# Optimization experiments

Hardware: AMD Instinct MI355X
Metric: run time of the kernel (lower is better)

The kernel has to match this reference:

```python
import jax, jax.numpy as jnp
import numpy as np
from jax import lax


def ternary_quant(w):
    # Layer-wise ternary quantization: alpha = mean(|w|), threshold = 0.001*alpha
    alpha = lax.stop_gradient(jnp.mean(jnp.abs(w)))
    thr = 0.001 * alpha
    q = jnp.where(w > thr, 1.0, jnp.where(w < -thr, -1.0, 0.0))
    return alpha * q


def setup_inputs() -> dict:
    key = jax.random.key(0)
    k1, k2, k3, k4, k5 = jax.random.split(key, 5)
    B, C, H, W = 32, 384, 64, 64
    fan_in = C * 3 * 3
    bound = 1.0 / np.sqrt(fan_in)  # torch Conv2d default init scale
    return {
        "x": jax.random.normal(k1, (B, C, H, W), dtype=jnp.float32),
        "weight": jax.random.uniform(k2, (C, C, 3, 3), dtype=jnp.float32, minval=-bound, maxval=bound),
        "bias": jax.random.uniform(k3, (C,), dtype=jnp.float32, minval=-bound, maxval=bound),
        "time_emb": jax.random.normal(k4, (B, 512), dtype=jnp.float32),
        "y": jax.random.randint(k5, (B,), 0, 1000, dtype=jnp.int64),
    }


def reference(x, weight, bias, time_emb, y):
    # time_emb and y are accepted but unused, matching Downsample.forward
    qw = ternary_quant(weight)
    out = lax.conv_general_dilated(
        x, qw,
        window_strides=(2, 2),
        padding=((1, 1), (1, 1)),
        dimension_numbers=("NCHW", "OIHW", "NCHW"),
    )
    return out + bias[None, :, None, None]
```

## Files before the change

### kernel.cpp

```cpp
#include <hip/hip_runtime.h>
#include <hip/hip_bf16.h>


#define CIN   384
#define HIN   64
#define WIN   64
#define OHW   32
#define KDIM  3456
#define NWELT 1327104
#define MDIM  32768

using bf16 = __hip_bfloat16;
typedef __attribute__((ext_vector_type(8))) short short8;
typedef __attribute__((ext_vector_type(4))) float floatx4;
typedef __attribute__((ext_vector_type(2))) unsigned short ushort2v;

#define AS1 __attribute__((address_space(1)))
#define AS3 __attribute__((address_space(3)))
#define DMA16(g, l) __builtin_amdgcn_global_load_lds((const AS1 void*)(g), (AS3 void*)(l), 16, 0, 0)

#define NPART  62
#define ZG_F   16
#define XN_OFF 256
#define WQ_OFF (256 + 100663296)

__global__ void absum_part(const float* __restrict__ w, float* __restrict__ ws) {
    const float4* w4 = (const float4*)w;
    float s = 0.f;
    for (int i = blockIdx.x * 256 + threadIdx.x; i < NWELT / 4; i += NPART * 256) {
        float4 v = w4[i];
        s += fabsf(v.x) + fabsf(v.y) + fabsf(v.z) + fabsf(v.w);
    }
    for (int off = 32; off; off >>= 1) s += __shfl_down(s, off, 64);
    __shared__ float red[4];
    if ((threadIdx.x & 63) == 0) red[threadIdx.x >> 6] = s;
    __syncthreads();
    if (threadIdx.x == 0) ws[2 + blockIdx.x] = red[0] + red[1] + red[2] + red[3];
}

__global__ void absum_final(float* __restrict__ ws) {
    if (threadIdx.x == 0) {
        float s = 0.f;
        for (int i = 0; i < NPART; ++i) s += ws[2 + i];
        float alpha = s * (1.0f / NWELT);
        ws[0] = alpha;
        ws[1] = 1e-3f * alpha;
        ws[ZG_F + 0] = 0.f; ws[ZG_F + 1] = 0.f;
        ws[ZG_F + 2] = 0.f; ws[ZG_F + 3] = 0.f;
    }
}

__global__ void quant_kernel(const float* __restrict__ w, const float* __restrict__ ws,
                             bf16* __restrict__ wq) {
    int j = blockIdx.x * 256 + threadIdx.x;
    if (j >= NWELT) return;
    float thr = ws[1];
    int o = j / KDIM;
    int rmd = j - o * KDIM;
    int khkw = rmd / 384;
    int c = rmd - khkw * 384;
    float v = w[((o * 384 + c) * 9) + khkw];
    float q = (v > thr) ? 1.f : ((v < -thr) ? -1.f : 0.f);
    wq[j] = __float2bfloat16(q);
}

__global__ void nhwc_kernel(const float* __restrict__ x, bf16* __restrict__ xn) {
    int nh = blockIdx.x;
    int n = nh >> 6, h = nh & 63;
    int c0 = blockIdx.y * 64;
    __shared__ bf16 tile[64][66];
    const float* src = x + ((n * CIN + c0) * HIN + h) * WIN;
    for (int i = 0; i < 4; ++i) {
        int s = threadIdx.x + i * 256;
        int cl = s >> 4, w4 = (s & 15) * 4;
        float4 v = *(const float4*)(src + cl * 4096 + w4);
        bf16 t0[2], t1[2];
        t0[0] = __float2bfloat16(v.x); t0[1] = __float2bfloat16(v.y);
        t1[0] = __float2bfloat16(v.z); t1[1] = __float2bfloat16(v.w);
        *(ushort2v*)&tile[cl][w4]     = *(ushort2v*)t0;
        *(ushort2v*)&tile[cl][w4 + 2] = *(ushort2v*)t1;
    }
    __syncthreads();
    bf16* dst = xn + ((size_t)(n * HIN + h) * WIN) * CIN + c0;
    for (int i = 0; i < 2; ++i) {
        int q = threadIdx.x + i * 256;
        int wc = q >> 3, c8 = (q & 7) * 8;
        bf16 tmp[8];
        #pragma unroll
        for (int j = 0; j < 8; ++j) tmp[j] = tile[c8 + j][wc];
        *(short8*)(dst + (size_t)wc * CIN + c8) = *(short8*)tmp;
    }
}

#define BM  128
#define BNO 128

__global__ __launch_bounds__(256) void conv_gemm(const bf16* __restrict__ xn,
                                                 const bf16* __restrict__ wq,
                                                 const float* __restrict__ ws,
                                                 const float* __restrict__ bias,
                                                 float* __restrict__ out,
                                                 const bf16* __restrict__ zg) {
    int m_base = blockIdx.x * BM;
    int o_base = blockIdx.y * BNO;
    __shared__ __align__(16) bf16 lW[BNO * 64];
    __shared__ __align__(16) bf16 lX[BM * 64];
    int tid = threadIdx.x;
    int lane = tid & 63;
    int wv = tid >> 6;
    int wo = (wv & 1) * 64;
    int wm = (wv >> 1) * 64;

    int g = (lane & 7) ^ (lane >> 3);
    const bf16* pw[4];
    const bf16* pxn[4];
    int oh2[4], ow2[4];
    bf16* ldsWb[4]; bf16* ldsXb[4];
    #pragma unroll
    for (int i = 0; i < 4; ++i) {
        int r = (wv * 4 + i) * 8 + (lane >> 3);
        ldsWb[i] = &lW[(wv * 4 + i) * 512];
        ldsXb[i] = &lX[(wv * 4 + i) * 512];
        pw[i] = wq + (size_t)(o_base + r) * KDIM + g * 8;
        int m = m_base + r;
        int n = m >> 10, oh = (m >> 5) & 31, ow = m & 31;
        pxn[i] = xn + (size_t)n * (HIN * WIN * CIN) + g * 8;
        oh2[i] = 2 * oh - 1;
        ow2[i] = 2 * ow - 1;
    }

    floatx4 acc[4][4];
    for (int i = 0; i < 4; ++i)
        for (int j = 0; j < 4; ++j)
            acc[i][j] = (floatx4){0.f, 0.f, 0.f, 0.f};

    for (int khkw = 0; khkw < 9; ++khkw) {
        int kh = khkw / 3, kw = khkw % 3;
        const bf16* pwk[4];
        const bf16* pxk[4];
        #pragma unroll
        for (int i = 0; i < 4; ++i) {
            pwk[i] = pw[i] + khkw * 384;
            int ih = oh2[i] + kh, iw = ow2[i] + kw;
            bool valid = (ih >= 0) & (iw >= 0);
            pxk[i] = valid ? pxn[i] + (ih * WIN + iw) * CIN : (const bf16*)0;
        }
        for (int cc = 0; cc < 6; ++cc) {
            int coff = cc * 64;
            #pragma unroll
            for (int i = 0; i < 4; ++i)
                DMA16(pwk[i] + coff, ldsWb[i]);
            #pragma unroll
            for (int i = 0; i < 4; ++i) {
                const bf16* p = pxk[i] ? pxk[i] + coff : zg;
                DMA16(p, ldsXb[i]);
            }
            __syncthreads();
            #pragma unroll
            for (int ks = 0; ks < 2; ++ks) {
                int oct = ((ks * 4 + (lane >> 4)) ^ (lane & 7)) * 8;
                short8 af[4], bfr[4];
                #pragma unroll
                for (int i = 0; i < 4; ++i)
                    af[i] = *(const short8*)(&lW[(wo + i * 16 + (lane & 15)) * 64 + oct]);
                #pragma unroll
                for (int j = 0; j < 4; ++j)
                    bfr[j] = *(const short8*)(&lX[(wm + j * 16 + (lane & 15)) * 64 + oct]);
                #pragma unroll
                for (int i = 0; i < 4; ++i)
                    #pragma unroll
                    for (int j = 0; j < 4; ++j)
                        acc[i][j] = __builtin_amdgcn_mfma_f32_16x16x32_bf16(af[i], bfr[j], acc[i][j], 0, 0, 0);
            }
            __syncthreads();
        }
    }

    float alpha = ws[0];
    int quad = lane >> 4, colm = lane & 15;
    for (int i = 0; i < 4; ++i) {
        for (int j = 0; j < 4; ++j) {
            int mm = m_base + wm + j * 16 + colm;
            int n = mm >> 10, oh = (mm >> 5) & 31, ow = mm & 31;
            for (int r = 0; r < 4; ++r) {
                int o = o_base + wo + i * 16 + quad * 4 + r;
                out[((n * 384 + o) * OHW + oh) * OHW + ow] = alpha * acc[i][j][r] + bias[o];
            }
        }
    }
}

extern "C" void kernel_launch(void* const* d_in, const int* in_sizes, int n_in,
                              void* d_out, int out_size, void* d_ws, size_t ws_size,
                              hipStream_t stream) {
    (void)in_sizes; (void)n_in; (void)out_size; (void)ws_size;
    const float* x    = (const float*)d_in[0];
    const float* w    = (const float*)d_in[1];
    const float* bias = (const float*)d_in[2];
    float* out = (float*)d_out;
    float* wsf = (float*)d_ws;
    bf16* xn = (bf16*)((char*)d_ws + XN_OFF);
    bf16* wq = (bf16*)((char*)d_ws + WQ_OFF);
    const bf16* zg = (const bf16*)(wsf + ZG_F);

    absum_part<<<NPART, 256, 0, stream>>>(w, wsf);
    absum_final<<<1, 64, 0, stream>>>(wsf);
    quant_kernel<<<(NWELT + 255) / 256, 256, 0, stream>>>(w, wsf, wq);
    nhwc_kernel<<<dim3(2048, 6), 256, 0, stream>>>(x, xn);
    conv_gemm<<<dim3(MDIM / BM, 384 / BNO), 256, 0, stream>>>(xn, wq, wsf, bias, out, zg);
}
```

Before: 427.7 us.

## Restructure conv GEMM into double-buffered 128x384 tile with interleaved DMA and MFMA

Each block of the implicit-GEMM conv kernel now covers all 384 output channels for 128 output pixels using 512 threads (8 waves), replacing the previous 128x128 tile grid. LDS is double-buffered, and global_load_lds prefetches of the next K-slice are interleaved with MFMA phases using explicit vmcnt waits, barriers and setprio. The aim is to reuse each input tile across all output channels, overlap memory traffic with compute, and reduce synchronisation stalls. In exchange it uses much more LDS per block and more accumulator registers, which can limit occupancy, and it depends on hand-tuned wait counts.

Result: no change. 426.3 us (-0.3%).

```diff
diff --git a/kernel.cpp b/kernel.cpp
--- a/kernel.cpp
+++ b/kernel.cpp
@@ -9,6 +9,7 @@
 #define KDIM  3456
 #define NWELT 1327104
 #define MDIM  32768
+#define NT    54
 
 using bf16 = __hip_bfloat16;
 typedef __attribute__((ext_vector_type(8))) short short8;
@@ -18,6 +19,12 @@
 #define AS1 __attribute__((address_space(1)))
 #define AS3 __attribute__((address_space(3)))
 #define DMA16(g, l) __builtin_amdgcn_global_load_lds((const AS1 void*)(g), (AS3 void*)(l), 16, 0, 0)
+
+#define EDGE(N) do { \
+    asm volatile("s_waitcnt vmcnt(" #N ")" ::: "memory"); \
+    __builtin_amdgcn_s_barrier(); \
+    __builtin_amdgcn_sched_barrier(0); \
+} while (0)
 
 #define NPART  62
 #define ZG_F   16
@@ -93,98 +100,257 @@
 }
 
 #define BM  128
-#define BNO 128
-
-__global__ __launch_bounds__(256) void conv_gemm(const bf16* __restrict__ xn,
-                                                 const bf16* __restrict__ wq,
-                                                 const float* __restrict__ ws,
-                                                 const float* __restrict__ bias,
-                                                 float* __restrict__ out,
-                                                 const bf16* __restrict__ zg) {
-    int m_base = blockIdx.x * BM;
-    int o_base = blockIdx.y * BNO;
-    __shared__ __align__(16) bf16 lW[BNO * 64];
-    __shared__ __align__(16) bf16 lX[BM * 64];
-    int tid = threadIdx.x;
-    int lane = tid & 63;
-    int wv = tid >> 6;
-    int wo = (wv & 1) * 64;
-    int wm = (wv >> 1) * 64;
-
-    int g = (lane & 7) ^ (lane >> 3);
-    const bf16* pw[4];
-    const bf16* pxn[4];
-    int oh2[4], ow2[4];
-    bf16* ldsWb[4]; bf16* ldsXb[4];
-    #pragma unroll
-    for (int i = 0; i < 4; ++i) {
-        int r = (wv * 4 + i) * 8 + (lane >> 3);
-        ldsWb[i] = &lW[(wv * 4 + i) * 512];
-        ldsXb[i] = &lX[(wv * 4 + i) * 512];
-        pw[i] = wq + (size_t)(o_base + r) * KDIM + g * 8;
-        int m = m_base + r;
+
+__global__ __launch_bounds__(512, 2) void conv_gemm(const bf16* __restrict__ xn,
+                                                    const bf16* __restrict__ wq,
+                                                    const float* __restrict__ ws,
+                                                    const float* __restrict__ bias,
+                                                    float* __restrict__ out,
+                                                    const bf16* __restrict__ zg) {
+    __shared__ __align__(16) bf16 lW[2][384 * 64];
+    __shared__ __align__(16) bf16 lX[2][128 * 64];
+    const int m_base = blockIdx.x * BM;
+    const int tid = threadIdx.x;
+    const int lane = tid & 63;
+    const int wv = tid >> 6;
+    const int io = wv & 3;
+    const int im = wv >> 2;
+    const int g = (lane & 7) ^ (lane >> 3);
+
+    const bf16* pw[2][3];
+    int wLoff[2][3];
+    #pragma unroll
+    for (int h = 0; h < 2; ++h)
+        #pragma unroll
+        for (int j = 0; j < 3; ++j) {
+            int rr = h * 192 + wv * 24 + j * 8;
+            pw[h][j] = wq + (size_t)(rr + (lane >> 3)) * KDIM + g * 8;
+            wLoff[h][j] = rr * 64;
+        }
+    const bf16* pxn[2];
+    int oh2[2], ow2[2], xLoff[2];
+    #pragma unroll
+    for (int h = 0; h < 2; ++h) {
+        int rr = h * 64 + wv * 8;
+        int m = m_base + rr + (lane >> 3);
         int n = m >> 10, oh = (m >> 5) & 31, ow = m & 31;
-        pxn[i] = xn + (size_t)n * (HIN * WIN * CIN) + g * 8;
-        oh2[i] = 2 * oh - 1;
-        ow2[i] = 2 * ow - 1;
-    }
-
-    floatx4 acc[4][4];
-    for (int i = 0; i < 4; ++i)
+        pxn[h] = xn + (size_t)n * (HIN * WIN * CIN) + g * 8;
+        oh2[h] = 2 * oh - 1;
+        ow2[h] = 2 * ow - 1;
+        xLoff[h] = rr * 64;
+    }
+
+    const int l15 = lane & 15, quad = lane >> 4, l7 = lane & 7;
+    const int octA = (quad ^ l7) * 8;
+    const int octB = ((4 + quad) ^ l7) * 8;
+    int aoff[2][3], boff[2][2];
+    #pragma unroll
+    for (int h = 0; h < 2; ++h)
+        #pragma unroll
+        for (int fo = 0; fo < 3; ++fo)
+            aoff[h][fo] = (h * 192 + io * 48 + fo * 16 + l15) * 64;
+    #pragma unroll
+    for (int h = 0; h < 2; ++h)
+        #pragma unroll
+        for (int fm = 0; fm < 2; ++fm)
+            boff[h][fm] = (h * 64 + im * 32 + fm * 16 + l15) * 64;
+
+    floatx4 acc[6][4];
+    #pragma unroll
+    for (int i = 0; i < 6; ++i)
+        #pragma unroll
         for (int j = 0; j < 4; ++j)
             acc[i][j] = (floatx4){0.f, 0.f, 0.f, 0.f};
 
-    for (int khkw = 0; khkw < 9; ++khkw) {
-        int kh = khkw / 3, kw = khkw % 3;
-        const bf16* pwk[4];
-        const bf16* pxk[4];
-        #pragma unroll
-        for (int i = 0; i < 4; ++i) {
-            pwk[i] = pw[i] + khkw * 384;
-            int ih = oh2[i] + kh, iw = ow2[i] + kw;
-            bool valid = (ih >= 0) & (iw >= 0);
-            pxk[i] = valid ? pxn[i] + (ih * WIN + iw) * CIN : (const bf16*)0;
-        }
-        for (int cc = 0; cc < 6; ++cc) {
-            int coff = cc * 64;
-            #pragma unroll
-            for (int i = 0; i < 4; ++i)
-                DMA16(pwk[i] + coff, ldsWb[i]);
-            #pragma unroll
-            for (int i = 0; i < 4; ++i) {
-                const bf16* p = pxk[i] ? pxk[i] + coff : zg;
-                DMA16(p, ldsXb[i]);
-            }
-            __syncthreads();
-            #pragma unroll
-            for (int ks = 0; ks < 2; ++ks) {
-                int oct = ((ks * 4 + (lane >> 4)) ^ (lane & 7)) * 8;
-                short8 af[4], bfr[4];
-                #pragma unroll
-                for (int i = 0; i < 4; ++i)
-                    af[i] = *(const short8*)(&lW[(wo + i * 16 + (lane & 15)) * 64 + oct]);
-                #pragma unroll
-                for (int j = 0; j < 4; ++j)
-                    bfr[j] = *(const short8*)(&lX[(wm + j * 16 + (lane & 15)) * 64 + oct]);
-                #pragma unroll
-                for (int i = 0; i < 4; ++i)
-                    #pragma unroll
-                    for (int j = 0; j < 4; ++j)
-                        acc[i][j] = __builtin_amdgcn_mfma_f32_16x16x32_bf16(af[i], bfr[j], acc[i][j], 0, 0, 0);
-            }
-            __syncthreads();
-        }
+    {
+        #pragma unroll
+        for (int j = 0; j < 3; ++j) DMA16(pw[0][j], &lW[0][wLoff[0][j]]);
+        {
+            int ih = oh2[0], iw = ow2[0];
+            const bf16* p = (ih >= 0 && iw >= 0) ? pxn[0] + (ih * WIN + iw) * CIN : zg;
+            DMA16(p, &lX[0][xLoff[0]]);
+        }
+        {
+            int ih = oh2[1], iw = ow2[1];
+            const bf16* p = (ih >= 0 && iw >= 0) ? pxn[1] + (ih * WIN + iw) * CIN : zg;
+            DMA16(p, &lX[0][xLoff[1]]);
+        }
+        #pragma unroll
+        for (int j = 0; j < 3; ++j) DMA16(pw[1][j], &lW[0][wLoff[1][j]]);
+        EDGE(4);
+    }
+
+    short8 af[2][3], bfl[2][2], bfh[2][2];
+
+    for (int t = 0; t < NT - 1; ++t) {
+        bf16* lWc = lW[t & 1];
+        bf16* lXc = lX[t & 1];
+        bf16* lWn = lW[(t & 1) ^ 1];
+        bf16* lXn = lX[(t & 1) ^ 1];
+        const int s = t + 1;
+        const int kk = s / 6, cs = s - kk * 6;
+        const int kh = kk / 3, kw = kk - kh * 3;
+        const int ws64 = s * 64;
+        const bf16* pxs[2];
+        #pragma unroll
+        for (int h = 0; h < 2; ++h) {
+            int ih = oh2[h] + kh, iw = ow2[h] + kw;
+            pxs[h] = (ih >= 0 && iw >= 0) ? pxn[h] + (ih * WIN + iw) * CIN + cs * 64 : zg;
+        }
+
+        #pragma unroll
+        for (int fo = 0; fo < 3; ++fo) {
+            af[0][fo] = *(const short8*)(lWc + aoff[0][fo] + octA);
+            af[1][fo] = *(const short8*)(lWc + aoff[0][fo] + octB);
+        }
+        #pragma unroll
+        for (int fm = 0; fm < 2; ++fm) {
+            bfl[0][fm] = *(const short8*)(lXc + boff[0][fm] + octA);
+            bfl[1][fm] = *(const short8*)(lXc + boff[0][fm] + octB);
+        }
+        #pragma unroll
+        for (int j = 0; j < 3; ++j) DMA16(pw[0][j] + ws64, lWn + wLoff[0][j]);
+        EDGE(6);
+        __builtin_amdgcn_s_setprio(1);
+        #pragma unroll
+        for (int ks = 0; ks < 2; ++ks)
+            #pragma unroll
+            for (int fo = 0; fo < 3; ++fo)
+                #pragma unroll
+                for (int fm = 0; fm < 2; ++fm)
+                    acc[fo][fm] = __builtin_amdgcn_mfma_f32_16x16x32_bf16(
+                        af[ks][fo], bfl[ks][fm], acc[fo][fm], 0, 0, 0);
+        __builtin_amdgcn_s_setprio(0);
+
+        #pragma unroll
+        for (int fm = 0; fm < 2; ++fm) {
+            bfh[0][fm] = *(const short8*)(lXc + boff[1][fm] + octA);
+            bfh[1][fm] = *(const short8*)(lXc + boff[1][fm] + octB);
+        }
+        DMA16(pxs[0], lXn + xLoff[0]);
+        EDGE(4);
+        __builtin_amdgcn_s_setprio(1);
+        #pragma unroll
+        for (int ks = 0; ks < 2; ++ks)
+            #pragma unroll
+            for (int fo = 0; fo < 3; ++fo)
+                #pragma unroll
+                for (int fm = 0; fm < 2; ++fm)
+                    acc[fo][2 + fm] = __builtin_amdgcn_mfma_f32_16x16x32_bf16(
+                        af[ks][fo], bfh[ks][fm], acc[fo][2 + fm], 0, 0, 0);
+        __builtin_amdgcn_s_setprio(0);
+
+        #pragma unroll
+        for (int fo = 0; fo < 3; ++fo) {
+            af[0][fo] = *(const short8*)(lWc + aoff[1][fo] + octA);
+            af[1][fo] = *(const short8*)(lWc + aoff[1][fo] + octB);
+        }
+        DMA16(pxs[1], lXn + xLoff[1]);
+        __builtin_amdgcn_s_setprio(1);
+        #pragma unroll
+        for (int ks = 0; ks < 2; ++ks)
+            #pragma unroll
+            for (int fo = 0; fo < 3; ++fo)
+                #pragma unroll
+                for (int fm = 0; fm < 2; ++fm)
+                    acc[3 + fo][2 + fm] = __builtin_amdgcn_mfma_f32_16x16x32_bf16(
+                        af[ks][fo], bfh[ks][fm], acc[3 + fo][2 + fm], 0, 0, 0);
+        __builtin_amdgcn_s_setprio(0);
+
+        #pragma unroll
+        for (int j = 0; j < 3; ++j) DMA16(pw[1][j] + ws64, lWn + wLoff[1][j]);
+        EDGE(4);
+        __builtin_amdgcn_s_setprio(1);
+        #pragma unroll
+        for (int ks = 0; ks < 2; ++ks)
+            #pragma unroll
+            for (int fo = 0; fo < 3; ++fo)
+                #pragma unroll
+                for (int fm = 0; fm < 2; ++fm)
+                    acc[3 + fo][fm] = __builtin_amdgcn_mfma_f32_16x16x32_bf16(
+                        af[ks][fo], bfl[ks][fm], acc[3 + fo][fm], 0, 0, 0);
+        __builtin_amdgcn_s_setprio(0);
+    }
+
+    {
+        bf16* lWc = lW[1];
+        bf16* lXc = lX[1];
+        #pragma unroll
+        for (int fo = 0; fo < 3; ++fo) {
+            af[0][fo] = *(const short8*)(lWc + aoff[0][fo] + octA);
+            af[1][fo] = *(const short8*)(lWc + aoff[0][fo] + octB);
+        }
+        #pragma unroll
+        for (int fm = 0; fm < 2; ++fm) {
+            bfl[0][fm] = *(const short8*)(lXc + boff[0][fm] + octA);
+            bfl[1][fm] = *(const short8*)(lXc + boff[0][fm] + octB);
+        }
+        EDGE(3);
+        __builtin_amdgcn_s_setprio(1);
+        #pragma unroll
+        for (int ks = 0; ks < 2; ++ks)
+            #pragma unroll
+            for (int fo = 0; fo < 3; ++fo)
+                #pragma unroll
+                for (int fm = 0; fm < 2; ++fm)
+                    acc[fo][fm] = __builtin_amdgcn_mfma_f32_16x16x32_bf16(
+                        af[ks][fo], bfl[ks][fm], acc[fo][fm], 0, 0, 0);
+        __builtin_amdgcn_s_setprio(0);
+        #pragma unroll
+        for (int fm = 0; fm < 2; ++fm) {
+            bfh[0][fm] = *(const short8*)(lXc + boff[1][fm] + octA);
+            bfh[1][fm] = *(const short8*)(lXc + boff[1][fm] + octB);
+        }
+        EDGE(0);
+        __builtin_amdgcn_s_setprio(1);
+        #pragma unroll
+        for (int ks = 0; ks < 2; ++ks)
+            #pragma unroll
+            for (int fo = 0; fo < 3; ++fo)
+                #pragma unroll
+                for (int fm = 0; fm < 2; ++fm)
+                    acc[fo][2 + fm] = __builtin_amdgcn_mfma_f32_16x16x32_bf16(
+                        af[ks][fo], bfh[ks][fm], acc[fo][2 + fm], 0, 0, 0);
+        __builtin_amdgcn_s_setprio(0);
+        #pragma unroll
+        for (int fo = 0; fo < 3; ++fo) {
+            af[0][fo] = *(const short8*)(lWc + aoff[1][fo] + octA);
+            af[1][fo] = *(const short8*)(lWc + aoff[1][fo] + octB);
+        }
+        __builtin_amdgcn_s_setprio(1);
+        #pragma unroll
+        for (int ks = 0; ks < 2; ++ks)
+            #pragma unroll
+            for (int fo = 0; fo < 3; ++fo)
+                #pragma unroll
+                for (int fm = 0; fm < 2; ++fm)
+                    acc[3 + fo][2 + fm] = __builtin_amdgcn_mfma_f32_16x16x32_bf16(
+                        af[ks][fo], bfh[ks][fm], acc[3 + fo][2 + fm], 0, 0, 0);
+        __builtin_amdgcn_s_setprio(0);
+        __builtin_amdgcn_s_setprio(1);
+        #pragma unroll
+        for (int ks = 0; ks < 2; ++ks)
+            #pragma unroll
+            for (int fo = 0; fo < 3; ++fo)
+                #pragma unroll
+                for (int fm = 0; fm < 2; ++fm)
+                    acc[3 + fo][fm] = __builtin_amdgcn_mfma_f32_16x16x32_bf16(
+                        af[ks][fo], bfl[ks][fm], acc[3 + fo][fm], 0, 0, 0);
+        __builtin_amdgcn_s_setprio(0);
     }
 
     float alpha = ws[0];
-    int quad = lane >> 4, colm = lane & 15;
-    for (int i = 0; i < 4; ++i) {
+    #pragma unroll
+    for (int i = 0; i < 6; ++i) {
+        int o0 = (i / 3) * 192 + io * 48 + (i % 3) * 16 + quad * 4;
+        #pragma unroll
         for (int j = 0; j < 4; ++j) {
-            int mm = m_base + wm + j * 16 + colm;
-            int n = mm >> 10, oh = (mm >> 5) & 31, ow = mm & 31;
+            int m = m_base + (j >> 1) * 64 + im * 32 + (j & 1) * 16 + l15;
+            int n = m >> 10, ohh = (m >> 5) & 31, oww = m & 31;
+            #pragma unroll
             for (int r = 0; r < 4; ++r) {
-                int o = o_base + wo + i * 16 + quad * 4 + r;
-                out[((n * 384 + o) * OHW + oh) * OHW + ow] = alpha * acc[i][j][r] + bias[o];
+                int o = o0 + r;
+                out[((n * 384 + o) * OHW + ohh) * OHW + oww] = alpha * acc[i][j][r] + bias[o];
             }
         }
     }
@@ -207,5 +373,5 @@
     absum_final<<<1, 64, 0, stream>>>(wsf);
     quant_kernel<<<(NWELT + 255) / 256, 256, 0, stream>>>(w, wsf, wq);
     nhwc_kernel<<<dim3(2048, 6), 256, 0, stream>>>(x, xn);
-    conv_gemm<<<dim3(MDIM / BM, 384 / BNO), 256, 0, stream>>>(xn, wq, wsf, bias, out, zg);
-}
+    conv_gemm<<<dim3(MDIM / BM, 1), 512, 0, stream>>>(xn, wq, wsf, bias, out, zg);
+}
```

## Software-pipeline conv GEMM with multi-buffered LDS and async DMA prefetch

Applied to the files above, without the earlier changes.

Restructures the implicit-GEMM main loop into a flattened 54-step pipeline with double-buffered weight tiles and triple-buffered activation tiles in LDS. Global-to-LDS loads for upcoming steps are issued before the MFMAs of the current step, and each step is closed by a single vmcnt wait plus barrier instead of two full syncthreads. Fragments are loaded into registers before the DMAs are issued, and MFMA issue priority is raised. This aims to hide memory latency behind compute, at the cost of more LDS (about 80KB per block) and more register pressure under launch_bounds(256,2).

New measurement: 444.5 us. 3.9% more time.

```diff
diff --git a/kernel.cpp b/kernel.cpp
--- a/kernel.cpp
+++ b/kernel.cpp
@@ -9,6 +9,7 @@
 #define KDIM  3456
 #define NWELT 1327104
 #define MDIM  32768
+#define NT    54
 
 using bf16 = __hip_bfloat16;
 typedef __attribute__((ext_vector_type(8))) short short8;
@@ -18,6 +19,12 @@
 #define AS1 __attribute__((address_space(1)))
 #define AS3 __attribute__((address_space(3)))
 #define DMA16(g, l) __builtin_amdgcn_global_load_lds((const AS1 void*)(g), (AS3 void*)(l), 16, 0, 0)
+
+#define EDGE_V(N) do { \
+    asm volatile("s_waitcnt vmcnt(" #N ")" ::: "memory"); \
+    __builtin_amdgcn_s_barrier(); \
+    __builtin_amdgcn_sched_barrier(0); \
+} while (0)
 
 #define NPART  62
 #define ZG_F   16
@@ -93,95 +100,150 @@
 }
 
 #define BM  128
-#define BNO 128
-
-__global__ __launch_bounds__(256) void conv_gemm(const bf16* __restrict__ xn,
-                                                 const bf16* __restrict__ wq,
-                                                 const float* __restrict__ ws,
-                                                 const float* __restrict__ bias,
-                                                 float* __restrict__ out,
-                                                 const bf16* __restrict__ zg) {
-    int m_base = blockIdx.x * BM;
-    int o_base = blockIdx.y * BNO;
-    __shared__ __align__(16) bf16 lW[BNO * 64];
-    __shared__ __align__(16) bf16 lX[BM * 64];
-    int tid = threadIdx.x;
-    int lane = tid & 63;
-    int wv = tid >> 6;
-    int wo = (wv & 1) * 64;
-    int wm = (wv >> 1) * 64;
-
-    int g = (lane & 7) ^ (lane >> 3);
+#define BN  128
+
+__global__ __launch_bounds__(256, 2) void conv_gemm(const bf16* __restrict__ xn,
+                                                    const bf16* __restrict__ wq,
+                                                    const float* __restrict__ ws,
+                                                    const float* __restrict__ bias,
+                                                    float* __restrict__ out,
+                                                    const bf16* __restrict__ zg) {
+    __shared__ __align__(16) bf16 lW[2][BN * 64];
+    __shared__ __align__(16) bf16 lX[3][BM * 64];
+    const int m_base = blockIdx.x * BM;
+    const int o_base = blockIdx.y * BN;
+    const int tid = threadIdx.x;
+    const int lane = tid & 63;
+    const int wv = tid >> 6;
+    const int wo = (wv & 1) * 64;
+    const int wm = (wv >> 1) * 64;
+    const int g = (lane & 7) ^ (lane >> 3);
+
     const bf16* pw[4];
     const bf16* pxn[4];
-    int oh2[4], ow2[4];
-    bf16* ldsWb[4]; bf16* ldsXb[4];
+    int oh2[4], ow2[4], wLoff[4], xLoff[4];
     #pragma unroll
     for (int i = 0; i < 4; ++i) {
-        int r = (wv * 4 + i) * 8 + (lane >> 3);
-        ldsWb[i] = &lW[(wv * 4 + i) * 512];
-        ldsXb[i] = &lX[(wv * 4 + i) * 512];
-        pw[i] = wq + (size_t)(o_base + r) * KDIM + g * 8;
-        int m = m_base + r;
+        int rr = (wv * 4 + i) * 8;
+        wLoff[i] = rr * 64;
+        xLoff[i] = rr * 64;
+        pw[i] = wq + (size_t)(o_base + rr + (lane >> 3)) * KDIM + g * 8;
+        int m = m_base + rr + (lane >> 3);
         int n = m >> 10, oh = (m >> 5) & 31, ow = m & 31;
         pxn[i] = xn + (size_t)n * (HIN * WIN * CIN) + g * 8;
         oh2[i] = 2 * oh - 1;
         ow2[i] = 2 * ow - 1;
     }
 
+    const int l15 = lane & 15, quad = lane >> 4, l7 = lane & 7;
+
     floatx4 acc[4][4];
+    #pragma unroll
     for (int i = 0; i < 4; ++i)
+        #pragma unroll
         for (int j = 0; j < 4; ++j)
             acc[i][j] = (floatx4){0.f, 0.f, 0.f, 0.f};
 
-    for (int khkw = 0; khkw < 9; ++khkw) {
-        int kh = khkw / 3, kw = khkw % 3;
-        const bf16* pwk[4];
-        const bf16* pxk[4];
+    {
         #pragma unroll
         for (int i = 0; i < 4; ++i) {
-            pwk[i] = pw[i] + khkw * 384;
-            int ih = oh2[i] + kh, iw = ow2[i] + kw;
-            bool valid = (ih >= 0) & (iw >= 0);
-            pxk[i] = valid ? pxn[i] + (ih * WIN + iw) * CIN : (const bf16*)0;
-        }
-        for (int cc = 0; cc < 6; ++cc) {
-            int coff = cc * 64;
-            #pragma unroll
-            for (int i = 0; i < 4; ++i)
-                DMA16(pwk[i] + coff, ldsWb[i]);
-            #pragma unroll
-            for (int i = 0; i < 4; ++i) {
-                const bf16* p = pxk[i] ? pxk[i] + coff : zg;
-                DMA16(p, ldsXb[i]);
-            }
-            __syncthreads();
-            #pragma unroll
-            for (int ks = 0; ks < 2; ++ks) {
-                int oct = ((ks * 4 + (lane >> 4)) ^ (lane & 7)) * 8;
-                short8 af[4], bfr[4];
-                #pragma unroll
-                for (int i = 0; i < 4; ++i)
-                    af[i] = *(const short8*)(&lW[(wo + i * 16 + (lane & 15)) * 64 + oct]);
+            int ih = oh2[i], iw = ow2[i];
+            const bf16* p = (ih >= 0 && iw >= 0) ? pxn[i] + (ih * WIN + iw) * CIN : zg;
+            DMA16(p, &lX[0][xLoff[i]]);
+        }
+        #pragma unroll
+        for (int i = 0; i < 4; ++i)
+            DMA16(pw[i], &lW[0][wLoff[i]]);
+        #pragma unroll
+        for (int i = 0; i < 4; ++i) {
+            int ih = oh2[i], iw = ow2[i];
+            const bf16* p = (ih >= 0 && iw >= 0) ? pxn[i] + (ih * WIN + iw) * CIN + 64 : zg;
+            DMA16(p, &lX[1][xLoff[i]]);
+        }
+        EDGE_V(4);
+    }
+
+    for (int t = 0; t < NT - 1; ++t) {
+        const bf16* lWc = lW[t & 1];
+        const bf16* lXc = lX[t % 3];
+        bf16* lWn = lW[(t + 1) & 1];
+        bf16* lXn2 = lX[(t + 2) % 3];
+        const int kW = (t + 1) * 64;
+        const int s2 = t + 2;
+        const int khkw2 = s2 / 6, cc2 = s2 - khkw2 * 6;
+        const int kh2 = khkw2 / 3, kw2 = khkw2 - kh2 * 3;
+
+        short8 af[2][4], bfr[2][4];
+        #pragma unroll
+        for (int ks = 0; ks < 2; ++ks) {
+            const int oct = ((ks * 4 + quad) ^ l7) * 8;
+            #pragma unroll
+            for (int i = 0; i < 4; ++i)
+                af[ks][i] = *(const short8*)(lWc + (wo + i * 16 + l15) * 64 + oct);
+            #pragma unroll
+            for (int j = 0; j < 4; ++j)
+                bfr[ks][j] = *(const short8*)(lXc + (wm + j * 16 + l15) * 64 + oct);
+        }
+
+        #pragma unroll
+        for (int i = 0; i < 4; ++i)
+            DMA16(pw[i] + kW, lWn + wLoff[i]);
+        #pragma unroll
+        for (int i = 0; i < 4; ++i) {
+            int ih = oh2[i] + kh2, iw = ow2[i] + kw2;
+            bool valid = (ih >= 0) & (iw >= 0) & (s2 < NT);
+            const bf16* p = valid ? pxn[i] + (ih * WIN + iw) * CIN + cc2 * 64 : zg;
+            DMA16(p, lXn2 + xLoff[i]);
+        }
+
+        __builtin_amdgcn_s_setprio(1);
+        #pragma unroll
+        for (int ks = 0; ks < 2; ++ks)
+            #pragma unroll
+            for (int i = 0; i < 4; ++i)
                 #pragma unroll
                 for (int j = 0; j < 4; ++j)
-                    bfr[j] = *(const short8*)(&lX[(wm + j * 16 + (lane & 15)) * 64 + oct]);
+                    acc[i][j] = __builtin_amdgcn_mfma_f32_16x16x32_bf16(
+                        af[ks][i], bfr[ks][j], acc[i][j], 0, 0, 0);
+        __builtin_amdgcn_s_setprio(0);
+
+        EDGE_V(4);
+    }
+
+    {
+        const bf16* lWc = lW[1];
+        const bf16* lXc = lX[53 % 3];
+        short8 af[2][4], bfr[2][4];
+        #pragma unroll
+        for (int ks = 0; ks < 2; ++ks) {
+            const int oct = ((ks * 4 + quad) ^ l7) * 8;
+            #pragma unroll
+            for (int i = 0; i < 4; ++i)
+                af[ks][i] = *(const short8*)(lWc + (wo + i * 16 + l15) * 64 + oct);
+            #pragma unroll
+            for (int j = 0; j < 4; ++j)
+                bfr[ks][j] = *(const short8*)(lXc + (wm + j * 16 + l15) * 64 + oct);
+        }
+        __builtin_amdgcn_s_setprio(1);
+        #pragma unroll
+        for (int ks = 0; ks < 2; ++ks)
+            #pragma unroll
+            for (int i = 0; i < 4; ++i)
                 #pragma unroll
-                for (int i = 0; i < 4; ++i)
-                    #pragma unroll
-                    for (int j = 0; j < 4; ++j)
-                        acc[i][j] = __builtin_amdgcn_mfma_f32_16x16x32_bf16(af[i], bfr[j], acc[i][j], 0, 0, 0);
-            }
-            __syncthreads();
-        }
+                for (int j = 0; j < 4; ++j)
+                    acc[i][j] = __builtin_amdgcn_mfma_f32_16x16x32_bf16(
+                        af[ks][i], bfr[ks][j], acc[i][j], 0, 0, 0);
+        __builtin_amdgcn_s_setprio(0);
     }
 
     float alpha = ws[0];
-    int quad = lane >> 4, colm = lane & 15;
+    #pragma unroll
     for (int i = 0; i < 4; ++i) {
+        #pragma unroll
         for (int j = 0; j < 4; ++j) {
-            int mm = m_base + wm + j * 16 + colm;
+            int mm = m_base + wm + j * 16 + l15;
             int n = mm >> 10, oh = (mm >> 5) & 31, ow = mm & 31;
+            #pragma unroll
             for (int r = 0; r < 4; ++r) {
                 int o = o_base + wo + i * 16 + quad * 4 + r;
                 out[((n * 384 + o) * OHW + oh) * OHW + ow] = alpha * acc[i][j][r] + bias[o];
@@ -207,5 +269,5 @@
     absum_final<<<1, 64, 0, stream>>>(wsf);
     quant_kernel<<<(NWELT + 255) / 256, 256, 0, stream>>>(w, wsf, wq);
     nhwc_kernel<<<dim3(2048, 6), 256, 0, stream>>>(x, xn);
-    conv_gemm<<<dim3(MDIM / BM, 384 / BNO), 256, 0, stream>>>(xn, wq, wsf, bias, out, zg);
-}
+    conv_gemm<<<dim3(MDIM / BM, 384 / BN), 256, 0, stream>>>(xn, wq, wsf, bias, out, zg);
+}
```
